# Performance work log

Hardware: AMD Instinct MI355X
Metric: run time of the kernel (lower is better)

The kernel has to match this reference:

```python
import jax, jax.numpy as jnp
import numpy as np

B, T, IN, H, L, OUT = 32, 512, 256, 1024, 2, 256


def setup_inputs() -> dict:
    key = jax.random.key(0)
    ks = jax.random.split(key, 12)
    s_in = 1.0 / np.sqrt(H)
    inp = {
        "input": jax.random.normal(ks[0], (B, T, IN), dtype=jnp.float32),
        # layer 0 GRU params (PyTorch layout: [3H, in], gate order r,z,n)
        "w_ih0": jax.random.uniform(ks[1], (3 * H, IN), jnp.float32, -s_in, s_in),
        "w_hh0": jax.random.uniform(ks[2], (3 * H, H), jnp.float32, -s_in, s_in),
        "b_ih0": jax.random.uniform(ks[3], (3 * H,), jnp.float32, -s_in, s_in),
        "b_hh0": jax.random.uniform(ks[4], (3 * H,), jnp.float32, -s_in, s_in),
        # layer 1 GRU params
        "w_ih1": jax.random.uniform(ks[5], (3 * H, H), jnp.float32, -s_in, s_in),
        "w_hh1": jax.random.uniform(ks[6], (3 * H, H), jnp.float32, -s_in, s_in),
        "b_ih1": jax.random.uniform(ks[7], (3 * H,), jnp.float32, -s_in, s_in),
        "b_hh1": jax.random.uniform(ks[8], (3 * H,), jnp.float32, -s_in, s_in),
        # final linear
        "fc_w": jax.random.uniform(ks[9], (OUT, H), jnp.float32, -s_in, s_in),
        "fc_b": jax.random.uniform(ks[10], (OUT,), jnp.float32, -s_in, s_in),
    }
    return inp


def _gru_layer(x, h0, w_ih, w_hh, b_ih, b_hh):
    # x: [B, T, D]; h0: [B, H]. Precompute all input projections at once.
    gx = jnp.einsum("btd,gd->btg", x, w_ih) + b_ih  # [B, T, 3H]

    def step(h, gx_t):
        gh = h @ w_hh.T + b_hh  # [B, 3H]
        xr, xz, xn = jnp.split(gx_t, 3, axis=-1)
        hr, hz, hn = jnp.split(gh, 3, axis=-1)
        r = jax.nn.sigmoid(xr + hr)
        z = jax.nn.sigmoid(xz + hz)
        n = jnp.tanh(xn + r * hn)
        h_new = (1.0 - z) * n + z * h
        return h_new, h_new

    h_last, hs = jax.lax.scan(step, h0, jnp.swapaxes(gx, 0, 1))  # hs: [T, B, H]
    return jnp.swapaxes(hs, 0, 1), h_last


def reference(input, w_ih0, w_hh0, b_ih0, b_hh0, w_ih1, w_hh1, b_ih1, b_hh1, fc_w, fc_b):
    b = input.shape[0]
    h0 = jnp.zeros((b, H), dtype=input.dtype)
    out0, h_last0 = _gru_layer(input, h0, w_ih0, w_hh0, b_ih0, b_hh0)
    out1, h_last1 = _gru_layer(out0, h0, w_ih1, w_hh1, b_ih1, b_hh1)
    h_n = jnp.stack([h_last0, h_last1], axis=0)  # [L, B, H]
    logits = out1[:, -1, :] @ fc_w.T + fc_b  # [B, OUT]
    return jax.nn.sigmoid(logits), h_n
```

## Files before the change

kernel.cpp:

```cpp
#include <hip/hip_runtime.h>

#define BB 32
#define TT 512
#define INW 256
#define HH 1024
#define OUTW 256
#define SLOT 32768

typedef __attribute__((ext_vector_type(8))) short short8;
typedef __attribute__((ext_vector_type(4))) float floatx4;
typedef __attribute__((ext_vector_type(4))) unsigned int uint4v;

#define SENT 0x7F807F80u

#define RSWZ(i) ((i) ^ ((((i) >> 5) & 3) << 2))

__device__ __forceinline__ unsigned short f2bf(float f) {
    unsigned int u = __float_as_uint(f);
    u = (u + 0x7fffu + ((u >> 16) & 1u)) >> 16;
    return (unsigned short)u;
}
__device__ __forceinline__ float bf2f(unsigned short h) {
    return __uint_as_float(((unsigned int)h) << 16);
}
__device__ __forceinline__ float fast_tanh(float x) {
    return 2.f / (1.f + __expf(-2.f * x)) - 1.f;
}
__device__ __forceinline__ float tree8(const float* p) {
    return ((p[0] + p[1]) + (p[2] + p[3])) + ((p[4] + p[5]) + (p[6] + p[7]));
}

__global__ void cast_f32_bf16(const float* __restrict__ src,
                              unsigned short* __restrict__ dst, int n) {
    int i = blockIdx.x * blockDim.x + threadIdx.x;
    int stride = gridDim.x * blockDim.x;
    for (; i < n; i += stride) dst[i] = f2bf(src[i]);
}

__global__ void fill_sent(uint4v* __restrict__ dst, size_t n4) {
    size_t i = (size_t)blockIdx.x * blockDim.x + threadIdx.x;
    size_t stride = (size_t)gridDim.x * blockDim.x;
    uint4v v = {SENT, SENT, SENT, SENT};
    for (; i < n4; i += stride) dst[i] = v;
}

template <int K>
__global__ __launch_bounds__(256) void gemm_gx(const unsigned short* __restrict__ X,
                                               const unsigned short* __restrict__ W,
                                               const float* __restrict__ bias,
                                               unsigned short* __restrict__ Cout) {
    __shared__ __align__(16) unsigned short As[64 * 40];
    __shared__ __align__(16) unsigned short Bs[64 * 40];
    int bid = blockIdx.x;
    int tn = bid % 48, tm = bid / 48;
    int tid = threadIdx.x;
    int lane = tid & 63, wv = tid >> 6;
    int wm = wv >> 1, wn = wv & 1;
    int l15 = lane & 15, q = lane >> 4;
    floatx4 acc[2][2] = {};
    int r = tid >> 2, kq = (tid & 3) * 8;
    const unsigned short* xrow = X + (size_t)(tm * 64 + r) * K;
    const unsigned short* wrow = W + (size_t)(tn * 64 + r) * K;
    const int NK = K / 32;
    for (int kk = 0; kk < NK; ++kk) {
        int k0 = kk * 32;
        *(short8*)&As[r * 40 + kq] = *(const short8*)&xrow[k0 + kq];
        *(short8*)&Bs[r * 40 + kq] = *(const short8*)&wrow[k0 + kq];
        __syncthreads();
        short8 a0 = *(const short8*)&As[(wm * 32 + l15) * 40 + q * 8];
        short8 a1 = *(const short8*)&As[(wm * 32 + 16 + l15) * 40 + q * 8];
        short8 b0 = *(const short8*)&Bs[(wn * 32 + l15) * 40 + q * 8];
        short8 b1 = *(const short8*)&Bs[(wn * 32 + 16 + l15) * 40 + q * 8];
        acc[0][0] = __builtin_amdgcn_mfma_f32_16x16x32_bf16(a0, b0, acc[0][0], 0, 0, 0);
        acc[0][1] = __builtin_amdgcn_mfma_f32_16x16x32_bf16(a0, b1, acc[0][1], 0, 0, 0);
        acc[1][0] = __builtin_amdgcn_mfma_f32_16x16x32_bf16(a1, b0, acc[1][0], 0, 0, 0);
        acc[1][1] = __builtin_amdgcn_mfma_f32_16x16x32_bf16(a1, b1, acc[1][1], 0, 0, 0);
        __syncthreads();
    }
    for (int mi = 0; mi < 2; ++mi)
        for (int ni = 0; ni < 2; ++ni) {
            int col = tn * 64 + wn * 32 + ni * 16 + l15;
            float bv = bias[col];
            int row0 = tm * 64 + wm * 32 + mi * 16 + q * 4;
            for (int rr = 0; rr < 4; ++rr) {
                Cout[(size_t)(row0 + rr) * 3072 + col] = f2bf(acc[mi][ni][rr] + bv);
            }
        }
}

__device__ __forceinline__ void probe_wait(const unsigned short* base, int wv3,
                                           int lane) {
    const unsigned int* pa =
        (const unsigned int*)base + (((wv3 << 4) + (lane & 15)) << 8) + 255;
    while (true) {
        unsigned int v;
        asm volatile("global_load_dword %0, %1, off sc0 sc1" : "=v"(v) : "v"(pa));
        asm volatile("s_waitcnt vmcnt(0)" : "+v"(v)::"memory");
        if (__all((int)(v != SENT))) break;
    }
}

__device__ __forceinline__ void spin_load8(const unsigned short* base, int kbase,
                                           int l15, int q, uint4v r0[8],
                                           uint4v r1[8]) {
    const unsigned short* ap[8];
#pragma unroll
    for (int s = 0; s < 8; ++s) {
        int k = kbase + s * 32 + q * 8;
        ap[s] = base + ((k >> 4) << 9) + (l15 << 4) + (k & 15);
    }
    while (true) {
#pragma unroll
        for (int s = 0; s < 8; ++s) {
            asm volatile("global_load_dwordx4 %0, %1, off sc0 sc1"
                         : "=&v"(r0[s]) : "v"(ap[s]));
            asm volatile("global_load_dwordx4 %0, %1, off offset:512 sc0 sc1"
                         : "=&v"(r1[s]) : "v"(ap[s]));
        }
        asm volatile("s_waitcnt vmcnt(0)"
                     : "+v"(r0[0]), "+v"(r0[1]), "+v"(r0[2]), "+v"(r0[3]),
                       "+v"(r0[4]), "+v"(r0[5]), "+v"(r0[6]), "+v"(r0[7]),
                       "+v"(r1[0]), "+v"(r1[1]), "+v"(r1[2]), "+v"(r1[3]),
                       "+v"(r1[4]), "+v"(r1[5]), "+v"(r1[6]), "+v"(r1[7])
                     :: "memory");
        unsigned bad = 0;
#pragma unroll
        for (int s = 0; s < 8; ++s) {
            bad |= (unsigned)(r0[s][0] == SENT) | (unsigned)(r0[s][1] == SENT) |
                   (unsigned)(r0[s][2] == SENT) | (unsigned)(r0[s][3] == SENT);
            bad |= (unsigned)(r1[s][0] == SENT) | (unsigned)(r1[s][1] == SENT) |
                   (unsigned)(r1[s][2] == SENT) | (unsigned)(r1[s][3] == SENT);
        }
        if (!__any((int)bad)) break;
    }
}

__device__ __forceinline__ void mfma8(const uint4v r0[8], const uint4v r1[8],
                                      const short8 Wr[8], const short8 Wz[8],
                                      const short8 Wn[8], floatx4 acc[6]) {
#pragma unroll
    for (int s = 0; s < 8; ++s) {
        short8 a0 = __builtin_bit_cast(short8, r0[s]);
        short8 a1 = __builtin_bit_cast(short8, r1[s]);
        acc[0] = __builtin_amdgcn_mfma_f32_16x16x32_bf16(a0, Wr[s], acc[0], 0, 0, 0);
        acc[1] = __builtin_amdgcn_mfma_f32_16x16x32_bf16(a0, Wz[s], acc[1], 0, 0, 0);
        acc[2] = __builtin_amdgcn_mfma_f32_16x16x32_bf16(a0, Wn[s], acc[2], 0, 0, 0);
        acc[3] = __builtin_amdgcn_mfma_f32_16x16x32_bf16(a1, Wr[s], acc[3], 0, 0, 0);
        acc[4] = __builtin_amdgcn_mfma_f32_16x16x32_bf16(a1, Wz[s], acc[4], 0, 0, 0);
        acc[5] = __builtin_amdgcn_mfma_f32_16x16x32_bf16(a1, Wn[s], acc[5], 0, 0, 0);
    }
}

__device__ __forceinline__ void hoist_w(const unsigned short* wsrc, int j0, int l15,
                                        int q, int kbase, short8 Wr[8], short8 Wz[8],
                                        short8 Wn[8]) {
    const unsigned short* w0 = wsrc + (size_t)(j0 + l15) * HH;
    const unsigned short* w1 = wsrc + (size_t)(1024 + j0 + l15) * HH;
    const unsigned short* w2 = wsrc + (size_t)(2048 + j0 + l15) * HH;
#pragma unroll
    for (int s = 0; s < 8; ++s) {
        int k = kbase + s * 32 + q * 8;
        Wr[s] = *(const short8*)&w0[k];
        Wz[s] = *(const short8*)&w1[k];
        Wn[s] = *(const short8*)&w2[k];
    }
}

__global__ __launch_bounds__(512) void gru_fused(
    const unsigned short* __restrict__ gx0, const unsigned short* __restrict__ whh0,
    const float* __restrict__ bhh0, const unsigned short* __restrict__ wih1,
    const unsigned short* __restrict__ whh1, const float* __restrict__ bih1,
    const float* __restrict__ bhh1, unsigned short* __restrict__ ring0,
    unsigned short* __restrict__ ring1, float* __restrict__ hn0,
    float* __restrict__ hn1) {
    __shared__ __align__(16) float red[8 * 6 * 64 * 4];
    const int bid = blockIdx.x;
    const int tid = threadIdx.x;
    const int lane = tid & 63, wv = tid >> 6;
    const int l15 = lane & 15, q = lane >> 4;
    const bool isGate = (wv >= 4);
    const int wv3 = wv & 3;
    const int gtid = tid & 255;
    const int gb = gtid >> 3, gjh = gtid & 7;
    const int gmi = gb >> 4, greg = gb & 3;
    const int grl = ((gb & 15) >> 2) * 16 + 2 * gjh;

    if (bid < 64) {
        const int j0 = bid * 16;
        const int kbase = wv3 * 256;
        short8 Wr[8], Wz[8], Wn[8];
        if (!isGate) hoist_w(whh0, j0, l15, q, kbase, Wr, Wz, Wn);

        float bR[2], bZ[2], bN[2], hpriv[2] = {0.f, 0.f};
        unsigned int pxr = 0, pxz = 0, pxn = 0;
        const unsigned short* gxp = nullptr;
        if (isGate) {
            int jj = j0 + 2 * gjh;
#pragma unroll
            for (int i = 0; i < 2; ++i) {
                bR[i] = bhh0[jj + i];
                bZ[i] = bhh0[1024 + jj + i];
                bN[i] = bhh0[2048 + jj + i];
            }
            gxp = gx0 + (size_t)gb * TT * 3072 + jj;
            pxr = *(const unsigned int*)(gxp);
            pxz = *(const unsigned int*)(gxp + 1024);
            pxn = *(const unsigned int*)(gxp + 2048);
        }

        for (int t = 0; t <= TT; ++t) {
            floatx4 acc[6] = {};
            bool doW = false;
            if (!isGate) {
                if (t < TT) {
                    const unsigned short* slot = ring0 + (size_t)t * SLOT;
                    probe_wait(slot, wv3, lane);
                    uint4v r0[8], r1[8];
                    spin_load8(slot, kbase, l15, q, r0, r1);
                    mfma8(r0, r1, Wr, Wz, Wn, acc);
                    doW = true;
                }
            } else if (t > 0) {
                unsigned int cxr = pxr, cxz = pxz, cxn = pxn;
                if (t < TT) {
                    const unsigned short* g2 = gxp + (size_t)t * 3072;
                    pxr = *(const unsigned int*)(g2);
                    pxz = *(const unsigned int*)(g2 + 1024);
                    pxn = *(const unsigned int*)(g2 + 2048);
                }
                float hnew[2];
#pragma unroll
                for (int i = 0; i < 2; ++i) {
                    int rl = grl + i;
                    float pr[4], pz[4], pn[4];
#pragma unroll
                    for (int w = 0; w < 4; ++w) {
                        pr[w] = red[RSWZ(((w * 6 + gmi * 3 + 0) * 64 + rl) * 4 + greg)];
                        pz[w] = red[RSWZ(((w * 6 + gmi * 3 + 1) * 64 + rl) * 4 + greg)];
                        pn[w] = red[RSWZ(((w * 6 + gmi * 3 + 2) * 64 + rl) * 4 + greg)];
                    }
                    float gr = (pr[0] + pr[1]) + (pr[2] + pr[3]);
                    float gz = (pz[0] + pz[1]) + (pz[2] + pz[3]);
                    float gn = (pn[0] + pn[1]) + (pn[2] + pn[3]);
                    float xr = bf2f((unsigned short)(i ? (cxr >> 16) : (cxr & 0xffffu)));
                    float xz = bf2f((unsigned short)(i ? (cxz >> 16) : (cxz & 0xffffu)));
                    float xn = bf2f((unsigned short)(i ? (cxn >> 16) : (cxn & 0xffffu)));
                    float rg = 1.f / (1.f + __expf(-(xr + gr + bR[i])));
                    float zg = 1.f / (1.f + __expf(-(xz + gz + bZ[i])));
                    float ng = fast_tanh(xn + rg * (gn + bN[i]));
                    hnew[i] = (1.f - zg) * ng + zg * hpriv[i];
                    hpriv[i] = hnew[i];
                }
                unsigned int hpack =
                    (unsigned int)f2bf(hnew[0]) | ((unsigned int)f2bf(hnew[1]) << 16);
                unsigned int* dst =
                    (unsigned int*)(ring0 + (size_t)t * SLOT) + (bid << 8) + gtid;
                __hip_atomic_store(dst, hpack, __ATOMIC_RELAXED,
                                   __HIP_MEMORY_SCOPE_AGENT);
                if (t == TT) {
                    hn0[gb * HH + j0 + 2 * gjh] = hnew[0];
                    hn0[gb * HH + j0 + 2 * gjh + 1] = hnew[1];
                }
            }
            __syncthreads();
            if (doW) {
#pragma unroll
                for (int tl = 0; tl < 6; ++tl)
                    *(floatx4*)&red[RSWZ(((wv3 * 6 + tl) * 64 + lane) * 4)] = acc[tl];
            }
            __syncthreads();
        }
    } else {
        const int b2 = bid - 64;
        const int j0 = b2 * 16;
        const int kbase = wv3 * 256;
        short8 Wr[8], Wz[8], Wn[8];
        hoist_w(isGate ? wih1 : whh1, j0, l15, q, kbase, Wr, Wz, Wn);

        float cR[2], cZ[2], cNx[2], cNh[2], hpriv[2] = {0.f, 0.f};
        if (isGate) {
            int jj = j0 + 2 * gjh;
#pragma unroll
            for (int i = 0; i < 2; ++i) {
                cR[i] = bih1[jj + i] + bhh1[jj + i];
                cZ[i] = bih1[1024 + jj + i] + bhh1[1024 + jj + i];
                cNx[i] = bih1[2048 + jj + i];
                cNh[i] = bhh1[2048 + jj + i];
            }
        }

        for (int t = 0; t <= TT; ++t) {
            floatx4 acc[6] = {};
            bool doW = false;
            if (!isGate) {
                if (t < TT) {
                    const unsigned short* slot = ring1 + (size_t)t * SLOT;
                    probe_wait(slot, wv3, lane);
                    uint4v r0[8], r1[8];
                    spin_load8(slot, kbase, l15, q, r0, r1);
                    mfma8(r0, r1, Wr, Wz, Wn, acc);
                    doW = true;
                }
            } else {
                if (t > 0) {
                    float hnew[2];
#pragma unroll
                    for (int i = 0; i < 2; ++i) {
                        int rl = grl + i;
                        float pr[8], pz[8], ph[4], px[4];
#pragma unroll
                        for (int w = 0; w < 8; ++w) {
                            pr[w] = red[RSWZ(((w * 6 + gmi * 3 + 0) * 64 + rl) * 4 + greg)];
                            pz[w] = red[RSWZ(((w * 6 + gmi * 3 + 1) * 64 + rl) * 4 + greg)];
                        }
#pragma unroll
                        for (int w = 0; w < 4; ++w)
                            ph[w] = red[RSWZ(((w * 6 + gmi * 3 + 2) * 64 + rl) * 4 + greg)];
#pragma unroll
                        for (int w = 4; w < 8; ++w)
                            px[w - 4] = red[RSWZ(((w * 6 + gmi * 3 + 2) * 64 + rl) * 4 + greg)];
                        float gr = tree8(pr), gz = tree8(pz);
                        float hn = (ph[0] + ph[1]) + (ph[2] + ph[3]);
                        float xn = (px[0] + px[1]) + (px[2] + px[3]);
                        float rg = 1.f / (1.f + __expf(-(gr + cR[i])));
                        float zg = 1.f / (1.f + __expf(-(gz + cZ[i])));
                        float ng = fast_tanh(xn + cNx[i] + rg * (hn + cNh[i]));
                        hnew[i] = (1.f - zg) * ng + zg * hpriv[i];
                        hpriv[i] = hnew[i];
                    }
                    unsigned int hpack =
                        (unsigned int)f2bf(hnew[0]) | ((unsigned int)f2bf(hnew[1]) << 16);
                    unsigned int* dst =
                        (unsigned int*)(ring1 + (size_t)t * SLOT) + (b2 << 8) + gtid;
                    __hip_atomic_store(dst, hpack, __ATOMIC_RELAXED,
                                       __HIP_MEMORY_SCOPE_AGENT);
                    if (t == TT) {
                        hn1[gb * HH + j0 + 2 * gjh] = hnew[0];
                        hn1[gb * HH + j0 + 2 * gjh + 1] = hnew[1];
                    }
                }
                if (t < TT) {
                    const unsigned short* slot = ring0 + (size_t)(t + 1) * SLOT;
                    probe_wait(slot, wv3, lane);
                    uint4v r0[8], r1[8];
                    spin_load8(slot, kbase, l15, q, r0, r1);
                    mfma8(r0, r1, Wr, Wz, Wn, acc);
                    doW = true;
                }
            }
            __syncthreads();
            if (doW) {
#pragma unroll
                for (int tl = 0; tl < 6; ++tl)
                    *(floatx4*)&red[RSWZ(((wv * 6 + tl) * 64 + lane) * 4)] = acc[tl];
            }
            __syncthreads();
        }
    }
}

__global__ void fc_out(const unsigned short* __restrict__ h1bf,
                       const float* __restrict__ fcw, const float* __restrict__ fcb,
                       float* __restrict__ out) {
    int b = blockIdx.x, o = threadIdx.x;
    const float* wr = fcw + (size_t)o * HH;
    float acc = fcb[o];
    for (int k = 0; k < HH; k += 16) {
        const unsigned short* hp = h1bf + ((k >> 4) << 9) + (b << 4);
#pragma unroll
        for (int i = 0; i < 16; ++i) acc += bf2f(hp[i]) * wr[k + i];
    }
    out[b * OUTW + o] = 1.f / (1.f + expf(-acc));
}

extern "C" void kernel_launch(void* const* d_in, const int* in_sizes, int n_in,
                              void* d_out, int out_size, void* d_ws, size_t ws_size,
                              hipStream_t stream) {
    (void)in_sizes; (void)n_in; (void)out_size; (void)ws_size;
    const float* input = (const float*)d_in[0];
    const float* w_ih0 = (const float*)d_in[1];
    const float* w_hh0 = (const float*)d_in[2];
    const float* b_ih0 = (const float*)d_in[3];
    const float* b_hh0 = (const float*)d_in[4];
    const float* w_ih1 = (const float*)d_in[5];
    const float* w_hh1 = (const float*)d_in[6];
    const float* b_ih1 = (const float*)d_in[7];
    const float* b_hh1 = (const float*)d_in[8];
    const float* fc_w = (const float*)d_in[9];
    const float* fc_b = (const float*)d_in[10];
    float* out = (float*)d_out;

    char* ws = (char*)d_ws;
    size_t off = 0;
    auto alloc = [&](size_t bytes) {
        void* p = ws + off;
        off += (bytes + 255) & ~(size_t)255;
        return p;
    };
    unsigned short* ring0 = (unsigned short*)alloc((size_t)(TT + 1) * SLOT * 2);
    unsigned short* ring1 = (unsigned short*)alloc((size_t)(TT + 1) * SLOT * 2);
    unsigned short* gx0 = (unsigned short*)alloc((size_t)16384 * 3072 * 2);
    unsigned short* in_bf = (unsigned short*)alloc((size_t)16384 * 256 * 2);
    unsigned short* wih0_bf = (unsigned short*)alloc((size_t)3072 * 256 * 2);
    unsigned short* whh0_bf = (unsigned short*)alloc((size_t)3072 * 1024 * 2);
    unsigned short* wih1_bf = (unsigned short*)alloc((size_t)3072 * 1024 * 2);
    unsigned short* whh1_bf = (unsigned short*)alloc((size_t)3072 * 1024 * 2);

    {
        size_t total_bytes = (size_t)2 * (TT + 1) * SLOT * 2;
        fill_sent<<<1024, 256, 0, stream>>>((uint4v*)ring0, total_bytes / 16);
    }

    cast_f32_bf16<<<256, 256, 0, stream>>>(input, in_bf, 16384 * 256);
    cast_f32_bf16<<<64, 256, 0, stream>>>(w_ih0, wih0_bf, 3072 * 256);
    cast_f32_bf16<<<256, 256, 0, stream>>>(w_hh0, whh0_bf, 3072 * 1024);
    cast_f32_bf16<<<256, 256, 0, stream>>>(w_ih1, wih1_bf, 3072 * 1024);
    cast_f32_bf16<<<256, 256, 0, stream>>>(w_hh1, whh1_bf, 3072 * 1024);

    hipMemsetAsync(ring0, 0, (size_t)SLOT * 2, stream);
    hipMemsetAsync(ring1, 0, (size_t)SLOT * 2, stream);

    gemm_gx<256><<<12288, 256, 0, stream>>>(in_bf, wih0_bf, b_ih0, gx0);

    gru_fused<<<128, 512, 0, stream>>>(gx0, whh0_bf, b_hh0, wih1_bf, whh1_bf, b_ih1,
                                       b_hh1, ring0, ring1, out + 8192,
                                       out + 8192 + 32768);

    fc_out<<<32, 256, 0, stream>>>(ring1 + (size_t)TT * SLOT, fc_w, fc_b, out);
}
```

Baseline: 2.213 ms.

## Stream ring loads in halves, fuse weight cast into hoist, raise gate priority

```diff
diff --git a/kernel.cpp b/kernel.cpp
--- a/kernel.cpp
+++ b/kernel.cpp
@@ -88,30 +88,18 @@
         }
 }
 
-__device__ __forceinline__ void probe_wait(const unsigned short* base, int wv3,
-                                           int lane) {
-    const unsigned int* pa =
-        (const unsigned int*)base + (((wv3 << 4) + (lane & 15)) << 8) + 255;
-    while (true) {
-        unsigned int v;
-        asm volatile("global_load_dword %0, %1, off sc0 sc1" : "=v"(v) : "v"(pa));
-        asm volatile("s_waitcnt vmcnt(0)" : "+v"(v)::"memory");
-        if (__all((int)(v != SENT))) break;
-    }
-}
-
-__device__ __forceinline__ void spin_load8(const unsigned short* base, int kbase,
-                                           int l15, int q, uint4v r0[8],
-                                           uint4v r1[8]) {
-    const unsigned short* ap[8];
-#pragma unroll
-    for (int s = 0; s < 8; ++s) {
+__device__ __forceinline__ void spin_load4(const unsigned short* base, int kbase,
+                                           int l15, int q, uint4v r0[4],
+                                           uint4v r1[4]) {
+    const unsigned short* ap[4];
+#pragma unroll
+    for (int s = 0; s < 4; ++s) {
         int k = kbase + s * 32 + q * 8;
         ap[s] = base + ((k >> 4) << 9) + (l15 << 4) + (k & 15);
     }
     while (true) {
 #pragma unroll
-        for (int s = 0; s < 8; ++s) {
+        for (int s = 0; s < 4; ++s) {
             asm volatile("global_load_dwordx4 %0, %1, off sc0 sc1"
                          : "=&v"(r0[s]) : "v"(ap[s]));
             asm volatile("global_load_dwordx4 %0, %1, off offset:512 sc0 sc1"
@@ -119,13 +107,11 @@
         }
         asm volatile("s_waitcnt vmcnt(0)"
                      : "+v"(r0[0]), "+v"(r0[1]), "+v"(r0[2]), "+v"(r0[3]),
-                       "+v"(r0[4]), "+v"(r0[5]), "+v"(r0[6]), "+v"(r0[7]),
-                       "+v"(r1[0]), "+v"(r1[1]), "+v"(r1[2]), "+v"(r1[3]),
-                       "+v"(r1[4]), "+v"(r1[5]), "+v"(r1[6]), "+v"(r1[7])
+                       "+v"(r1[0]), "+v"(r1[1]), "+v"(r1[2]), "+v"(r1[3])
                      :: "memory");
         unsigned bad = 0;
 #pragma unroll
-        for (int s = 0; s < 8; ++s) {
+        for (int s = 0; s < 4; ++s) {
             bad |= (unsigned)(r0[s][0] == SENT) | (unsigned)(r0[s][1] == SENT) |
                    (unsigned)(r0[s][2] == SENT) | (unsigned)(r0[s][3] == SENT);
             bad |= (unsigned)(r1[s][0] == SENT) | (unsigned)(r1[s][1] == SENT) |
@@ -135,11 +121,11 @@
     }
 }
 
-__device__ __forceinline__ void mfma8(const uint4v r0[8], const uint4v r1[8],
-                                      const short8 Wr[8], const short8 Wz[8],
-                                      const short8 Wn[8], floatx4 acc[6]) {
-#pragma unroll
-    for (int s = 0; s < 8; ++s) {
+__device__ __forceinline__ void mfma4(const uint4v r0[4], const uint4v r1[4],
+                                      const short8* Wr, const short8* Wz,
+                                      const short8* Wn, floatx4 acc[6]) {
+#pragma unroll
+    for (int s = 0; s < 4; ++s) {
         short8 a0 = __builtin_bit_cast(short8, r0[s]);
         short8 a1 = __builtin_bit_cast(short8, r1[s]);
         acc[0] = __builtin_amdgcn_mfma_f32_16x16x32_bf16(a0, Wr[s], acc[0], 0, 0, 0);
@@ -151,25 +137,42 @@
     }
 }
 
-__device__ __forceinline__ void hoist_w(const unsigned short* wsrc, int j0, int l15,
-                                        int q, int kbase, short8 Wr[8], short8 Wz[8],
-                                        short8 Wn[8]) {
-    const unsigned short* w0 = wsrc + (size_t)(j0 + l15) * HH;
-    const unsigned short* w1 = wsrc + (size_t)(1024 + j0 + l15) * HH;
-    const unsigned short* w2 = wsrc + (size_t)(2048 + j0 + l15) * HH;
+__device__ __forceinline__ void stream_mfma(const unsigned short* slot, int kbase,
+                                            int l15, int q, const short8 Wr[8],
+                                            const short8 Wz[8], const short8 Wn[8],
+                                            floatx4 acc[6]) {
+    uint4v r0[4], r1[4];
+    spin_load4(slot, kbase, l15, q, r0, r1);
+    mfma4(r0, r1, Wr, Wz, Wn, acc);
+    spin_load4(slot, kbase + 128, l15, q, r0, r1);
+    mfma4(r0, r1, Wr + 4, Wz + 4, Wn + 4, acc);
+}
+
+__device__ __forceinline__ short8 pack8(const float* p) {
+    short8 o;
+#pragma unroll
+    for (int i = 0; i < 8; ++i) o[i] = (short)f2bf(p[i]);
+    return o;
+}
+__device__ __forceinline__ void hoist_w_f32(const float* wsrc, int j0, int l15,
+                                            int q, int kbase, short8 Wr[8],
+                                            short8 Wz[8], short8 Wn[8]) {
+    const float* w0 = wsrc + (size_t)(j0 + l15) * HH;
+    const float* w1 = wsrc + (size_t)(1024 + j0 + l15) * HH;
+    const float* w2 = wsrc + (size_t)(2048 + j0 + l15) * HH;
 #pragma unroll
     for (int s = 0; s < 8; ++s) {
         int k = kbase + s * 32 + q * 8;
-        Wr[s] = *(const short8*)&w0[k];
-        Wz[s] = *(const short8*)&w1[k];
-        Wn[s] = *(const short8*)&w2[k];
+        Wr[s] = pack8(&w0[k]);
+        Wz[s] = pack8(&w1[k]);
+        Wn[s] = pack8(&w2[k]);
     }
 }
 
 __global__ __launch_bounds__(512) void gru_fused(
-    const unsigned short* __restrict__ gx0, const unsigned short* __restrict__ whh0,
-    const float* __restrict__ bhh0, const unsigned short* __restrict__ wih1,
-    const unsigned short* __restrict__ whh1, const float* __restrict__ bih1,
+    const unsigned short* __restrict__ gx0, const float* __restrict__ whh0,
+    const float* __restrict__ bhh0, const float* __restrict__ wih1,
+    const float* __restrict__ whh1, const float* __restrict__ bih1,
     const float* __restrict__ bhh1, unsigned short* __restrict__ ring0,
     unsigned short* __restrict__ ring1, float* __restrict__ hn0,
     float* __restrict__ hn1) {
@@ -189,7 +192,7 @@
         const int j0 = bid * 16;
         const int kbase = wv3 * 256;
         short8 Wr[8], Wz[8], Wn[8];
-        if (!isGate) hoist_w(whh0, j0, l15, q, kbase, Wr, Wz, Wn);
+        if (!isGate) hoist_w_f32(whh0, j0, l15, q, kbase, Wr, Wz, Wn);
 
         float bR[2], bZ[2], bN[2], hpriv[2] = {0.f, 0.f};
         unsigned int pxr = 0, pxz = 0, pxn = 0;
@@ -214,20 +217,12 @@
             if (!isGate) {
                 if (t < TT) {
                     const unsigned short* slot = ring0 + (size_t)t * SLOT;
-                    probe_wait(slot, wv3, lane);
-                    uint4v r0[8], r1[8];
-                    spin_load8(slot, kbase, l15, q, r0, r1);
-                    mfma8(r0, r1, Wr, Wz, Wn, acc);
+                    stream_mfma(slot, kbase, l15, q, Wr, Wz, Wn, acc);
                     doW = true;
                 }
             } else if (t > 0) {
+                __builtin_amdgcn_s_setprio(1);
                 unsigned int cxr = pxr, cxz = pxz, cxn = pxn;
-                if (t < TT) {
-                    const unsigned short* g2 = gxp + (size_t)t * 3072;
-                    pxr = *(const unsigned int*)(g2);
-                    pxz = *(const unsigned int*)(g2 + 1024);
-                    pxn = *(const unsigned int*)(g2 + 2048);
-                }
                 float hnew[2];
 #pragma unroll
                 for (int i = 0; i < 2; ++i) {
@@ -257,9 +252,16 @@
                     (unsigned int*)(ring0 + (size_t)t * SLOT) + (bid << 8) + gtid;
                 __hip_atomic_store(dst, hpack, __ATOMIC_RELAXED,
                                    __HIP_MEMORY_SCOPE_AGENT);
+                __builtin_amdgcn_s_setprio(0);
                 if (t == TT) {
                     hn0[gb * HH + j0 + 2 * gjh] = hnew[0];
                     hn0[gb * HH + j0 + 2 * gjh + 1] = hnew[1];
+                }
+                if (t < TT) {
+                    const unsigned short* g2 = gxp + (size_t)t * 3072;
+                    pxr = *(const unsigned int*)(g2);
+                    pxz = *(const unsigned int*)(g2 + 1024);
+                    pxn = *(const unsigned int*)(g2 + 2048);
                 }
             }
             __syncthreads();
@@ -275,7 +277,7 @@
         const int j0 = b2 * 16;
         const int kbase = wv3 * 256;
         short8 Wr[8], Wz[8], Wn[8];
-        hoist_w(isGate ? wih1 : whh1, j0, l15, q, kbase, Wr, Wz, Wn);
+        hoist_w_f32(isGate ? wih1 : whh1, j0, l15, q, kbase, Wr, Wz, Wn);
 
         float cR[2], cZ[2], cNx[2], cNh[2], hpriv[2] = {0.f, 0.f};
         if (isGate) {
@@ -295,14 +297,12 @@
             if (!isGate) {
                 if (t < TT) {
                     const unsigned short* slot = ring1 + (size_t)t * SLOT;
-                    probe_wait(slot, wv3, lane);
-                    uint4v r0[8], r1[8];
-                    spin_load8(slot, kbase, l15, q, r0, r1);
-                    mfma8(r0, r1, Wr, Wz, Wn, acc);
+                    stream_mfma(slot, kbase, l15, q, Wr, Wz, Wn, acc);
                     doW = true;
                 }
             } else {
                 if (t > 0) {
+                    __builtin_amdgcn_s_setprio(1);
                     float hnew[2];
 #pragma unroll
                     for (int i = 0; i < 2; ++i) {
@@ -334,6 +334,7 @@
                         (unsigned int*)(ring1 + (size_t)t * SLOT) + (b2 << 8) + gtid;
                     __hip_atomic_store(dst, hpack, __ATOMIC_RELAXED,
                                        __HIP_MEMORY_SCOPE_AGENT);
+                    __builtin_amdgcn_s_setprio(0);
                     if (t == TT) {
                         hn1[gb * HH + j0 + 2 * gjh] = hnew[0];
                         hn1[gb * HH + j0 + 2 * gjh + 1] = hnew[1];
@@ -341,10 +342,7 @@
                 }
                 if (t < TT) {
                     const unsigned short* slot = ring0 + (size_t)(t + 1) * SLOT;
-                    probe_wait(slot, wv3, lane);
-                    uint4v r0[8], r1[8];
-                    spin_load8(slot, kbase, l15, q, r0, r1);
-                    mfma8(r0, r1, Wr, Wz, Wn, acc);
+                    stream_mfma(slot, kbase, l15, q, Wr, Wz, Wn, acc);
                     doW = true;
                 }
             }
@@ -402,9 +400,6 @@
     unsigned short* gx0 = (unsigned short*)alloc((size_t)16384 * 3072 * 2);
     unsigned short* in_bf = (unsigned short*)alloc((size_t)16384 * 256 * 2);
     unsigned short* wih0_bf = (unsigned short*)alloc((size_t)3072 * 256 * 2);
-    unsigned short* whh0_bf = (unsigned short*)alloc((size_t)3072 * 1024 * 2);
-    unsigned short* wih1_bf = (unsigned short*)alloc((size_t)3072 * 1024 * 2);
-    unsigned short* whh1_bf = (unsigned short*)alloc((size_t)3072 * 1024 * 2);
 
     {
         size_t total_bytes = (size_t)2 * (TT + 1) * SLOT * 2;
@@ -413,16 +408,13 @@
 
     cast_f32_bf16<<<256, 256, 0, stream>>>(input, in_bf, 16384 * 256);
     cast_f32_bf16<<<64, 256, 0, stream>>>(w_ih0, wih0_bf, 3072 * 256);
-    cast_f32_bf16<<<256, 256, 0, stream>>>(w_hh0, whh0_bf, 3072 * 1024);
-    cast_f32_bf16<<<256, 256, 0, stream>>>(w_ih1, wih1_bf, 3072 * 1024);
-    cast_f32_bf16<<<256, 256, 0, stream>>>(w_hh1, whh1_bf, 3072 * 1024);
 
     hipMemsetAsync(ring0, 0, (size_t)SLOT * 2, stream);
     hipMemsetAsync(ring1, 0, (size_t)SLOT * 2, stream);
 
     gemm_gx<256><<<12288, 256, 0, stream>>>(in_bf, wih0_bf, b_ih0, gx0);
 
-    gru_fused<<<128, 512, 0, stream>>>(gx0, whh0_bf, b_hh0, wih1_bf, whh1_bf, b_ih1,
+    gru_fused<<<128, 512, 0, stream>>>(gx0, w_hh0, b_hh0, w_ih1, w_hh1, b_ih1,
                                        b_hh1, ring0, ring1, out + 8192,
                                        out + 8192 + 32768);
 
```

New measurement: 2.632 ms. 1.19x slower.
